# Performance work log

Hardware: AMD Instinct MI355X
Metric: run time of the kernel (lower is better)

The kernel has to match this reference:

```python
import jax, jax.numpy as jnp
import numpy as np

N, F, K, E = 50000, 128, 8, 1600000


def setup_inputs() -> dict:
    key = jax.random.key(0)
    k1, k2, k3, k4 = jax.random.split(key, 4)
    x = jax.random.normal(k1, (N, F), dtype=jnp.float32)
    adj = jax.random.randint(k2, (2, E), 0, N, dtype=jnp.int64)
    e = jax.random.normal(k3, (N, K), dtype=jnp.float32)
    stdv = 1.0 / np.sqrt(F)  # reset_parameters: uniform(-stdv, stdv)
    weights = jax.random.uniform(k4, (K, 2 * F, F), dtype=jnp.float32,
                                 minval=-stdv, maxval=stdv)
    return {"x": x, "adj": adj, "e": e, "weights": weights}


def _gcn_conv(x, row, col, n_nodes):
    # degree of each node as a message *destination* (col) -- matches torch degree(col, N)
    deg = jax.ops.segment_sum(jnp.ones(row.shape[0], x.dtype), col,
                              num_segments=n_nodes)
    val = (1.0 / jnp.sqrt(deg[col])) * (1.0 / jnp.sqrt(deg[row]))
    val = jnp.nan_to_num(val, nan=0.0, posinf=0.0, neginf=0.0)
    # SparseTensor(row=col, col=row) @ x : aggregate x[row] into col
    msg = val[:, None] * x[row]           # [E, F] gather
    return jax.ops.segment_sum(msg, col, num_segments=n_nodes)  # [N, F] scatter


def reference(x, adj, e, weights):
    n_nodes = x.shape[0]
    row, col = adj[0], adj[1]
    hi = _gcn_conv(x, row, col, n_nodes)                  # [N, F]
    hi = jnp.concatenate([hi, x], axis=1)                 # [N, 2F]
    # torch: repeat hi K times, bmm with [K,2F,F], transpose -> [N, K, F]
    outputs = jnp.einsum('nf,kfo->nko', hi, weights)      # [N, K, F]
    out = jnp.sum(e[:, :, None] * outputs, axis=1)        # gating sum over K
    out = out + x                                         # residual
    return out
```

## Files before the change

### kernel.cpp

```cpp
#include <hip/hip_runtime.h>
#include <hip/hip_bf16.h>

typedef __bf16 bf16_t;
typedef __bf16 bf16x8 __attribute__((ext_vector_type(8)));
typedef float f32x4 __attribute__((ext_vector_type(4)));

#define F 128
#define KEXP 8
#define BM 64
#define STG 8192

#define NB 196
#define CAP 12288
#define CH 8192

__global__ void k_initcur(int* __restrict__ cursor){
  int t = blockIdx.x*256 + threadIdx.x;
  if (t < NB) cursor[t] = t*CAP;
}

__global__ __launch_bounds__(256) void k_binA(const int* __restrict__ row,
    const int* __restrict__ col, int* __restrict__ cursor,
    int* __restrict__ region, int E){
  __shared__ int stage[CH];
  __shared__ unsigned char stageb[CH];
  __shared__ int hist[NB];
  __shared__ int lcur[NB];
  int tid = threadIdx.x;
  int base = blockIdx.x * CH;
  int cnt = min(CH, E - base);
  for (int i = tid; i < NB; i += 256) hist[i] = 0;
  __syncthreads();
  for (int i = tid; i < cnt; i += 256){
    int r = row[base+i], c = col[base+i];
    stage[i] = (r << 8) | (c & 255);
    stageb[i] = (unsigned char)(c >> 8);
    atomicAdd(&hist[c >> 8], 1);
  }
  __syncthreads();
  for (int i = tid; i < NB; i += 256)
    lcur[i] = atomicAdd(&cursor[i], hist[i]);
  __syncthreads();
  for (int i = tid; i < cnt; i += 256){
    int b = stageb[i];
    int pos = atomicAdd(&lcur[b], 1);
    region[pos] = stage[i];
  }
}

__global__ void k_bstart(const int* __restrict__ cursor, int* __restrict__ bstart,
                         int* __restrict__ offs, int Nn){
  __shared__ int lds[256];
  int t = threadIdx.x;
  int c = (t < NB) ? (cursor[t] - t*CAP) : 0;
  lds[t] = c; __syncthreads();
  for (int off=1; off<256; off<<=1){
    int u = (t>=off) ? lds[t-off] : 0;
    __syncthreads();
    lds[t] += u;
    __syncthreads();
  }
  if (t < NB) bstart[t] = lds[t] - c;
  if (t == NB-1){ bstart[NB] = lds[t]; offs[Nn] = lds[t]; }
}

__global__ __launch_bounds__(256) void k_binB(const int* __restrict__ region,
    const int* __restrict__ cursor, const int* __restrict__ bstart,
    int* __restrict__ deg, int* __restrict__ offs, int* __restrict__ bucket,
    int Nn){
  __shared__ int hist[256];
  __shared__ int loff[256];
  __shared__ int lcur[256];
  int b = blockIdx.x, t = threadIdx.x;
  int cnt = cursor[b] - b*CAP;
  const int* src = region + b*CAP;
  hist[t] = 0;
  __syncthreads();
  for (int i = t; i < cnt; i += 256) atomicAdd(&hist[src[i] & 255], 1);
  __syncthreads();
  int v = hist[t];
  loff[t] = v;
  __syncthreads();
  for (int off=1; off<256; off<<=1){
    int u = (t>=off) ? loff[t-off] : 0;
    __syncthreads();
    loff[t] += u;
    __syncthreads();
  }
  int excl = loff[t] - v;
  int gb = bstart[b];
  int node = b*256 + t;
  if (node < Nn){ deg[node] = v; offs[node] = gb + excl; }
  lcur[t] = gb + excl;
  __syncthreads();
  for (int i = t; i < cnt; i += 256){
    int p = src[i];
    int pos = atomicAdd(&lcur[p & 255], 1);
    bucket[pos] = p >> 8;
  }
}

__global__ void k_prep_xs(const float* __restrict__ x, const int* __restrict__ deg,
                          bf16_t* __restrict__ xs, int total8){
  int i = blockIdx.x*256 + threadIdx.x;
  if (i < total8){
    int n = i >> 4;
    int d = deg[n];
    float dr = d>0 ? rsqrtf((float)d) : 0.f;
    const float4 f0 = *reinterpret_cast<const float4*>(&x[i*8]);
    const float4 f1 = *reinterpret_cast<const float4*>(&x[i*8+4]);
    bf16x8 v;
    v[0]=(bf16_t)(dr*f0.x); v[1]=(bf16_t)(dr*f0.y);
    v[2]=(bf16_t)(dr*f0.z); v[3]=(bf16_t)(dr*f0.w);
    v[4]=(bf16_t)(dr*f1.x); v[5]=(bf16_t)(dr*f1.y);
    v[6]=(bf16_t)(dr*f1.z); v[7]=(bf16_t)(dr*f1.w);
    *reinterpret_cast<bf16x8*>(&xs[i*8]) = v;
  }
}

__global__ void k_prep_w(const float* __restrict__ W, bf16_t* __restrict__ Wt){
  int i8 = blockIdx.x*256 + threadIdx.x;
  if (i8 >= 32768) return;
  int st = i8 >> 10;
  int g  = i8 & 1023;
  int frag = g >> 6;
  int lane = g & 63;
  int h = st >> 4, kk = (st >> 1) & 7, s2 = st & 1;
  int sl = frag >> 3, cgg = frag & 7;
  int n = cgg*16 + (lane & 15);
  int fbase = h*128 + s2*64 + sl*32 + (lane >> 4)*8;
  bf16x8 v;
  #pragma unroll
  for (int j=0;j<8;j++)
    v[j] = (bf16_t)W[(size_t)kk*32768 + (size_t)(fbase+j)*128 + n];
  *reinterpret_cast<bf16x8*>(&Wt[(size_t)i8*8]) = v;
}

__global__ __launch_bounds__(256) void k_agg(const bf16_t* __restrict__ xs,
    const int* __restrict__ offs, const int* __restrict__ bucket,
    bf16_t* __restrict__ hi, int Nn){
  int wid = threadIdx.x >> 6, lane = threadIdx.x & 63;
  int n = blockIdx.x*4 + wid;
  if (n >= Nn) return;
  int g = lane >> 4, j16 = lane & 15;
  int o0 = offs[n], o1 = offs[n+1];
  float acc[8] = {0.f,0.f,0.f,0.f,0.f,0.f,0.f,0.f};
  int j = o0 + g;
  for (; j + 12 < o1; j += 16){
    int r0 = bucket[j];
    int r1 = bucket[j+4];
    int r2 = bucket[j+8];
    int r3 = bucket[j+12];
    bf16x8 v0 = *reinterpret_cast<const bf16x8*>(&xs[(size_t)r0*F + j16*8]);
    bf16x8 v1 = *reinterpret_cast<const bf16x8*>(&xs[(size_t)r1*F + j16*8]);
    bf16x8 v2 = *reinterpret_cast<const bf16x8*>(&xs[(size_t)r2*F + j16*8]);
    bf16x8 v3 = *reinterpret_cast<const bf16x8*>(&xs[(size_t)r3*F + j16*8]);
    #pragma unroll
    for (int i=0;i<8;i++)
      acc[i] += ((float)v0[i] + (float)v1[i]) + ((float)v2[i] + (float)v3[i]);
  }
  for (; j < o1; j += 4){
    int r0 = bucket[j];
    bf16x8 v0 = *reinterpret_cast<const bf16x8*>(&xs[(size_t)r0*F + j16*8]);
    #pragma unroll
    for (int i=0;i<8;i++) acc[i] += (float)v0[i];
  }
  #pragma unroll
  for (int i=0;i<8;i++){
    acc[i] += __shfl_down(acc[i], 32);
    acc[i] += __shfl_down(acc[i], 16);
  }
  if (g == 0){
    int dn = o1 - o0;
    float dc = dn>0 ? rsqrtf((float)dn) : 0.f;
    bf16x8 o;
    #pragma unroll
    for (int i=0;i<8;i++) o[i] = (bf16_t)(dc*acc[i]);
    *reinterpret_cast<bf16x8*>(&hi[(size_t)n*F + j16*8]) = o;
  }
}

#define MFMA_BF16 __builtin_amdgcn_mfma_f32_16x16x32_bf16

__global__ __launch_bounds__(256) void k_gemm(
    const bf16_t* __restrict__ hi, const float* __restrict__ x,
    const float* __restrict__ e, const bf16_t* __restrict__ Wt,
    float* __restrict__ out, int Nn)
{
  __shared__ float e_s[BM*KEXP];
  int tid = threadIdx.x;
  int base = blockIdx.x * BM;
  int lane = tid & 63, wid = tid >> 6;
  int rw = wid >> 1, cw = wid & 1;
  int r16 = lane & 15, kc = lane >> 4;

  if (tid < 128){
    int row = tid >> 1;
    int srow = min(base + row, Nn-1);
    *reinterpret_cast<float4*>(&e_s[tid*4]) =
      *reinterpret_cast<const float4*>(&e[(size_t)srow*KEXP + (tid&1)*4]);
  }

  int rA = min(base + rw*32 + r16,      Nn-1);
  int rB = min(base + rw*32 + 16 + r16, Nn-1);
  bf16x8 a[2][4];
  #pragma unroll
  for (int fi=0; fi<4; fi++){
    a[0][fi] = *reinterpret_cast<const bf16x8*>(&hi[(size_t)rA*F + fi*32 + kc*8]);
    a[1][fi] = *reinterpret_cast<const bf16x8*>(&hi[(size_t)rB*F + fi*32 + kc*8]);
  }

  const bf16_t* wbase = Wt + (size_t)(cw*4)*512 + (size_t)lane*8;
  bf16x8 bc[2][4], bn[2][4];
  #pragma unroll
  for (int sl=0; sl<2; sl++)
    #pragma unroll
    for (int cg=0; cg<4; cg++)
      bc[sl][cg] = *reinterpret_cast<const bf16x8*>(&wbase[(size_t)(sl*8+cg)*512]);

  __syncthreads();

  f32x4 acc[2][4], ck[2][4];
  #pragma unroll
  for (int rg=0;rg<2;rg++)
    #pragma unroll
    for (int cg=0;cg<4;cg++){
      acc[rg][cg] = (f32x4){0.f,0.f,0.f,0.f};
      ck[rg][cg]  = (f32x4){0.f,0.f,0.f,0.f};
    }

  for (int sp=0; sp<16; sp++){
    if (sp == 8){
      #pragma unroll
      for (int fi=0; fi<4; fi++){
        const float4 f0 = *reinterpret_cast<const float4*>(&x[(size_t)rA*F + fi*32 + kc*8]);
        const float4 f1 = *reinterpret_cast<const float4*>(&x[(size_t)rA*F + fi*32 + kc*8 + 4]);
        bf16x8 v;
        v[0]=(bf16_t)f0.x; v[1]=(bf16_t)f0.y; v[2]=(bf16_t)f0.z; v[3]=(bf16_t)f0.w;
        v[4]=(bf16_t)f1.x; v[5]=(bf16_t)f1.y; v[6]=(bf16_t)f1.z; v[7]=(bf16_t)f1.w;
        a[0][fi] = v;
        const float4 g0 = *reinterpret_cast<const float4*>(&x[(size_t)rB*F + fi*32 + kc*8]);
        const float4 g1 = *reinterpret_cast<const float4*>(&x[(size_t)rB*F + fi*32 + kc*8 + 4]);
        bf16x8 u;
        u[0]=(bf16_t)g0.x; u[1]=(bf16_t)g0.y; u[2]=(bf16_t)g0.z; u[3]=(bf16_t)g0.w;
        u[4]=(bf16_t)g1.x; u[5]=(bf16_t)g1.y; u[6]=(bf16_t)g1.z; u[7]=(bf16_t)g1.w;
        a[1][fi] = u;
      }
    }

    {
      const bf16_t* wn = wbase + (size_t)(2*sp+1)*STG;
      #pragma unroll
      for (int sl=0; sl<2; sl++)
        #pragma unroll
        for (int cg=0; cg<4; cg++)
          bn[sl][cg] = *reinterpret_cast<const bf16x8*>(&wn[(size_t)(sl*8+cg)*512]);
      #pragma unroll
      for (int sl=0; sl<2; sl++)
        #pragma unroll
        for (int cg=0; cg<4; cg++){
          ck[0][cg] = MFMA_BF16(a[0][sl], bc[sl][cg], ck[0][cg], 0, 0, 0);
          ck[1][cg] = MFMA_BF16(a[1][sl], bc[sl][cg], ck[1][cg], 0, 0, 0);
        }
    }
    {
      if (sp < 15){
        const bf16_t* wn = wbase + (size_t)(2*sp+2)*STG;
        #pragma unroll
        for (int sl=0; sl<2; sl++)
          #pragma unroll
          for (int cg=0; cg<4; cg++)
            bc[sl][cg] = *reinterpret_cast<const bf16x8*>(&wn[(size_t)(sl*8+cg)*512]);
      }
      #pragma unroll
      for (int sl=0; sl<2; sl++)
        #pragma unroll
        for (int cg=0; cg<4; cg++){
          ck[0][cg] = MFMA_BF16(a[0][2+sl], bn[sl][cg], ck[0][cg], 0, 0, 0);
          ck[1][cg] = MFMA_BF16(a[1][2+sl], bn[sl][cg], ck[1][cg], 0, 0, 0);
        }
      int kk = sp & 7;
      float ev[2][4];
      #pragma unroll
      for (int rg=0;rg<2;rg++)
        #pragma unroll
        for (int r=0;r<4;r++)
          ev[rg][r] = e_s[(rw*32 + rg*16 + kc*4 + r)*KEXP + kk];
      #pragma unroll
      for (int rg=0;rg<2;rg++)
        #pragma unroll
        for (int cg=0;cg<4;cg++){
          #pragma unroll
          for (int r=0;r<4;r++)
            acc[rg][cg][r] += ev[rg][r]*ck[rg][cg][r];
          ck[rg][cg] = (f32x4){0.f,0.f,0.f,0.f};
        }
    }
  }

  #pragma unroll
  for (int rg=0;rg<2;rg++){
    #pragma unroll
    for (int cg=0; cg<4; cg++){
      int ocol = cw*64 + cg*16 + r16;
      #pragma unroll
      for (int r=0; r<4; r++){
        int node = base + rw*32 + rg*16 + kc*4 + r;
        if (node < Nn)
          out[(size_t)node*F + ocol] = acc[rg][cg][r] + x[(size_t)node*F + ocol];
      }
    }
  }
}

extern "C" void kernel_launch(void* const* d_in, const int* in_sizes, int n_in,
                              void* d_out, int out_size, void* d_ws, size_t ws_size,
                              hipStream_t stream){
  const float* x  = (const float*)d_in[0];
  const int*  adj = (const int*)d_in[1];
  const float* e  = (const float*)d_in[2];
  const float* W  = (const float*)d_in[3];
  float* out = (float*)d_out;
  int Nn = in_sizes[0] / F;
  int E  = in_sizes[1] / 2;
  const int* rowp = adj;
  const int* colp = adj + E;

  char* w = (char*)d_ws;
  auto alloc = [&](size_t b){ char* p = w; w += (b + 255) & ~(size_t)255; return p; };
  int* deg     = (int*)alloc((size_t)Nn*4);
  int* offs    = (int*)alloc(((size_t)Nn+1)*4);
  int* cursor  = (int*)alloc((size_t)NB*4);
  int* bstart  = (int*)alloc((size_t)(NB+1)*4);
  int* bucket  = (int*)alloc((size_t)E*4);
  char* uni    = alloc((size_t)Nn*F*2 > (size_t)NB*CAP*4 ? (size_t)Nn*F*2
                                                          : (size_t)NB*CAP*4);
  int* region  = (int*)uni;
  bf16_t* xs   = (bf16_t*)uni;
  bf16_t* hi   = (bf16_t*)alloc((size_t)Nn*F*2);
  bf16_t* Wt   = (bf16_t*)alloc((size_t)2048*F*2);

  int nchunks = (E + CH - 1) / CH;
  k_initcur<<<1, 256, 0, stream>>>(cursor);
  k_binA<<<nchunks, 256, 0, stream>>>(rowp, colp, cursor, region, E);
  k_bstart<<<1, 256, 0, stream>>>(cursor, bstart, offs, Nn);
  k_binB<<<NB, 256, 0, stream>>>(region, cursor, bstart, deg, offs, bucket, Nn);
  k_prep_xs<<<(Nn*F/8+255)/256, 256, 0, stream>>>(x, deg, xs, Nn*F/8);
  k_prep_w<<<(32768+255)/256, 256, 0, stream>>>(W, Wt);
  k_agg<<<(Nn+3)/4, 256, 0, stream>>>(xs, offs, bucket, hi, Nn);
  k_gemm<<<(Nn+BM-1)/BM, 256, 0, stream>>>(hi, x, e, Wt, out, Nn);
}
```

Baseline: 165.1 us.

## Restructure gated GEMM so each wave covers all rows and a 32-column slice

Changes the k_gemm warp tiling so each of the four waves handles all 64 rows and a 32-column output slice, instead of a 2x2 split of 32 rows by 64 columns. The K reduction is reorganised into 32 stages that step through expert and K-half. The weight prep kernel is re-laid out to match the new stage order, and the gating coefficients are stored transposed in shared memory so each lane reads them as one vector. The intent is to cut register pressure and per-wave weight traffic and to simplify the gating update. The cost is reloading the A fragments four times instead of twice, plus possible exposed latency from the new loop structure.

```diff
diff --git a/kernel.cpp b/kernel.cpp
--- a/kernel.cpp
+++ b/kernel.cpp
@@ -125,7 +125,7 @@
   int g  = i8 & 1023;
   int frag = g >> 6;
   int lane = g & 63;
-  int h = st >> 4, kk = (st >> 1) & 7, s2 = st & 1;
+  int h = st >> 4, s2 = (st >> 3) & 1, kk = st & 7;
   int sl = frag >> 3, cgg = frag & 7;
   int n = cgg*16 + (lane & 15);
   int fbase = h*128 + s2*64 + sl*32 + (lane >> 4)*8;
@@ -187,125 +187,125 @@
     const float* __restrict__ e, const bf16_t* __restrict__ Wt,
     float* __restrict__ out, int Nn)
 {
-  __shared__ float e_s[BM*KEXP];
+  __shared__ float e_sT[KEXP*BM];
   int tid = threadIdx.x;
   int base = blockIdx.x * BM;
   int lane = tid & 63, wid = tid >> 6;
-  int rw = wid >> 1, cw = wid & 1;
   int r16 = lane & 15, kc = lane >> 4;
 
-  if (tid < 128){
-    int row = tid >> 1;
+  for (int i = tid; i < KEXP*BM; i += 256){
+    int kk = i & 7, row = i >> 3;
     int srow = min(base + row, Nn-1);
-    *reinterpret_cast<float4*>(&e_s[tid*4]) =
-      *reinterpret_cast<const float4*>(&e[(size_t)srow*KEXP + (tid&1)*4]);
-  }
-
-  int rA = min(base + rw*32 + r16,      Nn-1);
-  int rB = min(base + rw*32 + 16 + r16, Nn-1);
-  bf16x8 a[2][4];
-  #pragma unroll
-  for (int fi=0; fi<4; fi++){
-    a[0][fi] = *reinterpret_cast<const bf16x8*>(&hi[(size_t)rA*F + fi*32 + kc*8]);
-    a[1][fi] = *reinterpret_cast<const bf16x8*>(&hi[(size_t)rB*F + fi*32 + kc*8]);
-  }
-
-  const bf16_t* wbase = Wt + (size_t)(cw*4)*512 + (size_t)lane*8;
-  bf16x8 bc[2][4], bn[2][4];
+    e_sT[kk*BM + row] = e[(size_t)srow*KEXP + kk];
+  }
+
+  int rr[4];
+  #pragma unroll
+  for (int rg=0; rg<4; rg++) rr[rg] = min(base + rg*16 + r16, Nn-1);
+
+  bf16x8 a[4][2];
+  #pragma unroll
+  for (int rg=0; rg<4; rg++)
+    #pragma unroll
+    for (int sl=0; sl<2; sl++)
+      a[rg][sl] = *reinterpret_cast<const bf16x8*>(
+          &hi[(size_t)rr[rg]*F + sl*32 + kc*8]);
+
+  const bf16_t* wb = Wt + (size_t)(wid*2)*512 + (size_t)lane*8;
+  bf16x8 bc[2][2], bn[2][2];
   #pragma unroll
   for (int sl=0; sl<2; sl++)
     #pragma unroll
-    for (int cg=0; cg<4; cg++)
-      bc[sl][cg] = *reinterpret_cast<const bf16x8*>(&wbase[(size_t)(sl*8+cg)*512]);
-
-  __syncthreads();
-
-  f32x4 acc[2][4], ck[2][4];
-  #pragma unroll
-  for (int rg=0;rg<2;rg++)
-    #pragma unroll
-    for (int cg=0;cg<4;cg++){
-      acc[rg][cg] = (f32x4){0.f,0.f,0.f,0.f};
-      ck[rg][cg]  = (f32x4){0.f,0.f,0.f,0.f};
+    for (int cg=0; cg<2; cg++)
+      bc[sl][cg] = *reinterpret_cast<const bf16x8*>(&wb[(size_t)(sl*8+cg)*512]);
+
+  __syncthreads();
+
+  f32x4 acc[4][2];
+  #pragma unroll
+  for (int rg=0;rg<4;rg++)
+    #pragma unroll
+    for (int cg=0;cg<2;cg++) acc[rg][cg] = (f32x4){0.f,0.f,0.f,0.f};
+
+  #pragma unroll 2
+  for (int st=0; st<32; st++){
+    if (st == 8){
+      #pragma unroll
+      for (int rg=0; rg<4; rg++)
+        #pragma unroll
+        for (int sl=0; sl<2; sl++)
+          a[rg][sl] = *reinterpret_cast<const bf16x8*>(
+              &hi[(size_t)rr[rg]*F + 64 + sl*32 + kc*8]);
+    } else if (st == 16 || st == 24){
+      int off = (st == 16) ? 0 : 64;
+      #pragma unroll
+      for (int rg=0; rg<4; rg++)
+        #pragma unroll
+        for (int sl=0; sl<2; sl++){
+          const float4 f0 = *reinterpret_cast<const float4*>(
+              &x[(size_t)rr[rg]*F + off + sl*32 + kc*8]);
+          const float4 f1 = *reinterpret_cast<const float4*>(
+              &x[(size_t)rr[rg]*F + off + sl*32 + kc*8 + 4]);
+          bf16x8 v;
+          v[0]=(bf16_t)f0.x; v[1]=(bf16_t)f0.y; v[2]=(bf16_t)f0.z; v[3]=(bf16_t)f0.w;
+          v[4]=(bf16_t)f1.x; v[5]=(bf16_t)f1.y; v[6]=(bf16_t)f1.z; v[7]=(bf16_t)f1.w;
+          a[rg][sl] = v;
+        }
     }
 
-  for (int sp=0; sp<16; sp++){
-    if (sp == 8){
-      #pragma unroll
-      for (int fi=0; fi<4; fi++){
-        const float4 f0 = *reinterpret_cast<const float4*>(&x[(size_t)rA*F + fi*32 + kc*8]);
-        const float4 f1 = *reinterpret_cast<const float4*>(&x[(size_t)rA*F + fi*32 + kc*8 + 4]);
-        bf16x8 v;
-        v[0]=(bf16_t)f0.x; v[1]=(bf16_t)f0.y; v[2]=(bf16_t)f0.z; v[3]=(bf16_t)f0.w;
-        v[4]=(bf16_t)f1.x; v[5]=(bf16_t)f1.y; v[6]=(bf16_t)f1.z; v[7]=(bf16_t)f1.w;
-        a[0][fi] = v;
-        const float4 g0 = *reinterpret_cast<const float4*>(&x[(size_t)rB*F + fi*32 + kc*8]);
-        const float4 g1 = *reinterpret_cast<const float4*>(&x[(size_t)rB*F + fi*32 + kc*8 + 4]);
-        bf16x8 u;
-        u[0]=(bf16_t)g0.x; u[1]=(bf16_t)g0.y; u[2]=(bf16_t)g0.z; u[3]=(bf16_t)g0.w;
-        u[4]=(bf16_t)g1.x; u[5]=(bf16_t)g1.y; u[6]=(bf16_t)g1.z; u[7]=(bf16_t)g1.w;
-        a[1][fi] = u;
+    if (st < 31){
+      const bf16_t* wn = wb + (size_t)(st+1)*STG;
+      #pragma unroll
+      for (int sl=0; sl<2; sl++)
+        #pragma unroll
+        for (int cg=0; cg<2; cg++)
+          bn[sl][cg] = *reinterpret_cast<const bf16x8*>(
+              &wn[(size_t)(sl*8+cg)*512]);
+    }
+
+    f32x4 ck[4][2];
+    #pragma unroll
+    for (int rg=0;rg<4;rg++)
+      #pragma unroll
+      for (int cg=0;cg<2;cg++) ck[rg][cg] = (f32x4){0.f,0.f,0.f,0.f};
+    #pragma unroll
+    for (int sl=0; sl<2; sl++)
+      #pragma unroll
+      for (int cg=0; cg<2; cg++)
+        #pragma unroll
+        for (int rg=0; rg<4; rg++)
+          ck[rg][cg] = MFMA_BF16(a[rg][sl], bc[sl][cg], ck[rg][cg], 0, 0, 0);
+
+    {
+      int kk = st & 7;
+      #pragma unroll
+      for (int rg=0; rg<4; rg++){
+        f32x4 ev = *reinterpret_cast<const f32x4*>(
+            &e_sT[kk*BM + rg*16 + kc*4]);
+        #pragma unroll
+        for (int cg=0; cg<2; cg++){
+          #pragma unroll
+          for (int r=0; r<4; r++)
+            acc[rg][cg][r] += ev[r]*ck[rg][cg][r];
+        }
       }
     }
 
-    {
-      const bf16_t* wn = wbase + (size_t)(2*sp+1)*STG;
-      #pragma unroll
-      for (int sl=0; sl<2; sl++)
-        #pragma unroll
-        for (int cg=0; cg<4; cg++)
-          bn[sl][cg] = *reinterpret_cast<const bf16x8*>(&wn[(size_t)(sl*8+cg)*512]);
-      #pragma unroll
-      for (int sl=0; sl<2; sl++)
-        #pragma unroll
-        for (int cg=0; cg<4; cg++){
-          ck[0][cg] = MFMA_BF16(a[0][sl], bc[sl][cg], ck[0][cg], 0, 0, 0);
-          ck[1][cg] = MFMA_BF16(a[1][sl], bc[sl][cg], ck[1][cg], 0, 0, 0);
-        }
-    }
-    {
-      if (sp < 15){
-        const bf16_t* wn = wbase + (size_t)(2*sp+2)*STG;
-        #pragma unroll
-        for (int sl=0; sl<2; sl++)
-          #pragma unroll
-          for (int cg=0; cg<4; cg++)
-            bc[sl][cg] = *reinterpret_cast<const bf16x8*>(&wn[(size_t)(sl*8+cg)*512]);
-      }
-      #pragma unroll
-      for (int sl=0; sl<2; sl++)
-        #pragma unroll
-        for (int cg=0; cg<4; cg++){
-          ck[0][cg] = MFMA_BF16(a[0][2+sl], bn[sl][cg], ck[0][cg], 0, 0, 0);
-          ck[1][cg] = MFMA_BF16(a[1][2+sl], bn[sl][cg], ck[1][cg], 0, 0, 0);
-        }
-      int kk = sp & 7;
-      float ev[2][4];
-      #pragma unroll
-      for (int rg=0;rg<2;rg++)
-        #pragma unroll
-        for (int r=0;r<4;r++)
-          ev[rg][r] = e_s[(rw*32 + rg*16 + kc*4 + r)*KEXP + kk];
-      #pragma unroll
-      for (int rg=0;rg<2;rg++)
-        #pragma unroll
-        for (int cg=0;cg<4;cg++){
-          #pragma unroll
-          for (int r=0;r<4;r++)
-            acc[rg][cg][r] += ev[rg][r]*ck[rg][cg][r];
-          ck[rg][cg] = (f32x4){0.f,0.f,0.f,0.f};
-        }
-    }
-  }
-
-  #pragma unroll
-  for (int rg=0;rg<2;rg++){
-    #pragma unroll
-    for (int cg=0; cg<4; cg++){
-      int ocol = cw*64 + cg*16 + r16;
+    #pragma unroll
+    for (int sl=0; sl<2; sl++)
+      #pragma unroll
+      for (int cg=0; cg<2; cg++)
+        bc[sl][cg] = bn[sl][cg];
+  }
+
+  #pragma unroll
+  for (int rg=0; rg<4; rg++){
+    #pragma unroll
+    for (int cg=0; cg<2; cg++){
+      int ocol = wid*32 + cg*16 + r16;
       #pragma unroll
       for (int r=0; r<4; r++){
-        int node = base + rw*32 + rg*16 + kc*4 + r;
+        int node = base + rg*16 + kc*4 + r;
         if (node < Nn)
           out[(size_t)node*F + ocol] = acc[rg][cg][r] + x[(size_t)node*F + ocol];
       }
```

Result: slower. 173.4 us (+5.0%).
